# Performance work log

Measured on AMD Instinct MI355X. Metric: run time of the kernel, lower is better.

Reference implementation:

```python
import jax, jax.numpy as jnp
import numpy as np

LEAKY = 0.2  # tf.nn.leaky_relu default alpha
E_SZ = [64, 64, 16]
F_SZ = [128, 128, 8]
N_MAPS, C, H, W = 64, 1, 32, 32
B = 8192


def _leaky(x):
    return jnp.where(x >= 0, x, LEAKY * x)


def func_theta(x, theta, sz, in_sz):
    # x: [B, in_sz]; theta: [B, total]; per-sample MLP with weights sliced from theta
    y = x
    offset = 0
    n = len(sz)
    for i, out_sz in enumerate(sz):
        w_sz = in_sz * out_sz
        Wm = theta[:, offset:offset + w_sz].reshape(-1, in_sz, out_sz)
        offset += w_sz
        b = theta[:, offset:offset + out_sz]
        offset += out_sz
        y = jnp.einsum('bi,bio->bo', y, Wm) + b
        if i < n - 1:
            y = _leaky(y)
        in_sz = out_sz
    return y


def setup_inputs() -> dict:
    key = jax.random.key(0)
    ks = jax.random.split(key, 16)

    def g(k, shape, scale):
        return (jax.random.normal(k, shape, dtype=jnp.float32) * scale)

    inp = {
        'indices': jax.random.randint(ks[0], (B,), 0, N_MAPS, dtype=jnp.int32),
        'states': jax.random.normal(ks[1], (B, 4), dtype=jnp.float32),
        'maps': jax.random.normal(ks[2], (N_MAPS, C, H, W), dtype=jnp.float32),
        'fc1_w': g(ks[3], (C * H * W, 256), 1.0 / np.sqrt(C * H * W)),
        'fc1_b': jnp.zeros((256,), jnp.float32),
        'fc2_w': g(ks[4], (256, 128), 1.0 / np.sqrt(256)),
        'fc2_b': jnp.zeros((128,), jnp.float32),
        'fc3_w': g(ks[5], (128, 128), 1.0 / np.sqrt(128)),
        'fc3_b': jnp.zeros((128,), jnp.float32),
        'bn_w': g(ks[6], (128, 32), 1.0 / np.sqrt(128)),
        'bn_b': jnp.zeros((32,), jnp.float32),
        'e_w': g(ks[7], (32, 5456), 1e-5),
        'e_b': g(ks[8], (5456,), 1e-3),
        'f_w': g(ks[9], (32, 21768), 1e-5),
        'f_b': g(ks[10], (21768,), 1e-3),
    }
    return inp


def reference(indices, states, maps, fc1_w, fc1_b, fc2_w, fc2_b, fc3_w, fc3_b,
              bn_w, bn_b, e_w, e_b, f_w, f_b):
    # gather maps per sample and flatten (NCHW -> NHWC transpose is a no-op after flatten
    # mathematically, but keep the exact data layout of the original)
    m = jnp.transpose(maps[indices], (0, 2, 3, 1)).astype(jnp.float32)  # [B,H,W,C]
    z = m.reshape(m.shape[0], -1)

    # hypernet trunk
    z = _leaky(z @ fc1_w + fc1_b)
    z = _leaky(z @ fc2_w + fc2_b)
    z = _leaky(z @ fc3_w + fc3_b)
    z = z @ bn_w + bn_b  # bottleneck, no activation
    theta_e = z @ e_w + e_b  # [B, 5456]
    theta_f = z @ f_w + f_b  # [B, 21768]

    S = states[:, 0:2]
    G = states[:, 2:4]
    e_s = func_theta(S, theta_e, E_SZ, 2)
    e_g = func_theta(G, theta_e, E_SZ, 2)
    zf = jnp.concatenate([e_s, e_g], axis=-1)  # [B, 32]
    ang = func_theta(zf, theta_f, F_SZ, 2 * E_SZ[-1])  # [B, 8]
    pts = jnp.concatenate([jnp.sin(ang), jnp.cos(ang)], axis=-1)  # [B, 16]
    return pts
```

## Files before the change

### kernel.cpp

```cpp
#include <hip/hip_runtime.h>
#include <hip/hip_bf16.h>


#define LEAKY 0.2f
#define NCLS 64
#define B_TOT 8192
#define NSLICE 4


__device__ __forceinline__ float lrelu(float x) { return x >= 0.f ? x : LEAKY * x; }

__global__ __launch_bounds__(1024) void backbone_bucket_kernel(
    const float* __restrict__ maps,
    const float* __restrict__ fc1_w, const float* __restrict__ fc1_b,
    const float* __restrict__ fc2_w, const float* __restrict__ fc2_b,
    const float* __restrict__ fc3_w, const float* __restrict__ fc3_b,
    const float* __restrict__ bn_w,  const float* __restrict__ bn_b,
    float* __restrict__ z,
    const int* __restrict__ idx, int* __restrict__ counts,
    int* __restrict__ offsets, int* __restrict__ perm)
{
    __shared__ float m[1024];
    __shared__ float red[1024];
    __shared__ float h1[256];
    __shared__ float h2[128];
    __shared__ float h3[128];
    __shared__ int cnt[16][64];
    __shared__ int wcur[16][64];

    const int t = threadIdx.x;

    if (blockIdx.x == 64) {
        const int w = t >> 6;
        cnt[w][t & 63] = 0;
        __syncthreads();
        int my[8];
#pragma unroll
        for (int r = 0; r < 8; ++r) {
            my[r] = idx[r * 1024 + t];
            atomicAdd(&cnt[w][my[r]], 1);
        }
        __syncthreads();
        if (t < 64) {
            int run = 0;
#pragma unroll
            for (int w2 = 0; w2 < 16; ++w2) {
                const int v = cnt[w2][t];
                wcur[w2][t] = run;
                run += v;
            }
            counts[t] = run;
            int x = run;
            for (int d = 1; d < 64; d <<= 1) {
                const int y = __shfl_up(x, d, 64);
                if (t >= d) x += y;
            }
            const int basec = x - run;
            offsets[t] = basec;
#pragma unroll
            for (int w2 = 0; w2 < 16; ++w2) wcur[w2][t] += basec;
        }
        __syncthreads();
#pragma unroll
        for (int r = 0; r < 8; ++r) {
            const int p = atomicAdd(&wcur[w][my[r]], 1);
            perm[p] = r * 1024 + t;
        }
        return;
    }

    const int c = blockIdx.x;
    m[t] = maps[(size_t)c * 1024 + t];
    __syncthreads();

    {
        const int o = t & 255, ks = t >> 8;
        const float* wp = fc1_w + o;
        float acc = 0.f;
#pragma unroll 8
        for (int i = 0; i < 256; ++i) {
            const int k = ks * 256 + i;
            acc += m[k] * wp[(size_t)k * 256];
        }
        red[t] = acc;
    }
    __syncthreads();
    if (t < 256)
        h1[t] = lrelu(fc1_b[t] + red[t] + red[256 + t] + red[512 + t] + red[768 + t]);
    __syncthreads();
    {
        const int o = t & 127, ks = t >> 7;
        float acc = 0.f;
#pragma unroll
        for (int i = 0; i < 32; ++i) {
            const int k = ks * 32 + i;
            acc += h1[k] * fc2_w[k * 128 + o];
        }
        red[t] = acc;
    }
    __syncthreads();
    if (t < 128) {
        float a = fc2_b[t];
#pragma unroll
        for (int r = 0; r < 8; ++r) a += red[r * 128 + t];
        h2[t] = lrelu(a);
    }
    __syncthreads();
    {
        const int o = t & 127, ks = t >> 7;
        float acc = 0.f;
#pragma unroll
        for (int i = 0; i < 16; ++i) {
            const int k = ks * 16 + i;
            acc += h2[k] * fc3_w[k * 128 + o];
        }
        red[t] = acc;
    }
    __syncthreads();
    if (t < 128) {
        float a = fc3_b[t];
#pragma unroll
        for (int r = 0; r < 8; ++r) a += red[r * 128 + t];
        h3[t] = lrelu(a);
    }
    __syncthreads();
    {
        const int o = t & 31, ks = t >> 5;
        float acc = 0.f;
#pragma unroll
        for (int i = 0; i < 4; ++i) {
            const int k = ks * 4 + i;
            acc += h3[k] * bn_w[k * 32 + o];
        }
        red[t] = acc;
    }
    __syncthreads();
    if (t < 32) {
        float a = bn_b[t];
#pragma unroll
        for (int r = 0; r < 32; ++r) a += red[r * 32 + t];
        z[c * 32 + t] = a;
    }
}

__global__ __launch_bounds__(256) void theta_kernel(
    const float* __restrict__ z,
    const float* __restrict__ e_w, const float* __restrict__ e_b,
    const float* __restrict__ f_w, const float* __restrict__ f_b,
    float* __restrict__ th_e, float* __restrict__ th_f)
{
    __shared__ __align__(16) float zl[2048];
    const int t = threadIdx.x;
    ((float4*)zl)[t]       = ((const float4*)z)[t];
    ((float4*)zl)[t + 256] = ((const float4*)z)[t + 256];
    __syncthreads();

    int j = blockIdx.x * 256 + t;
    const int cbase = blockIdx.y * 8;
    const float* wbase;
    float* op;
    int stride;
    float bias;
    if (j < 5456) {
        wbase = e_w + j; bias = e_b[j]; op = th_e + j; stride = 5456;
    } else {
        const int jj = j - 5456;
        if (jj >= 21768) return;
        wbase = f_w + jj; bias = f_b[jj]; op = th_f + jj; stride = 21768;
    }
    float wk[32];
#pragma unroll
    for (int k = 0; k < 32; ++k) wk[k] = wbase[(size_t)k * stride];

#pragma unroll
    for (int cc = 0; cc < 8; cc += 4) {
        const int c0 = cbase + cc;
        float a0 = bias, a1 = bias, a2 = bias, a3 = bias;
#pragma unroll
        for (int k4 = 0; k4 < 8; ++k4) {
            const float4 z0 = *(const float4*)&zl[(c0 + 0) * 32 + k4 * 4];
            const float4 z1 = *(const float4*)&zl[(c0 + 1) * 32 + k4 * 4];
            const float4 z2 = *(const float4*)&zl[(c0 + 2) * 32 + k4 * 4];
            const float4 z3 = *(const float4*)&zl[(c0 + 3) * 32 + k4 * 4];
            const float w0 = wk[k4 * 4], w1 = wk[k4 * 4 + 1];
            const float w2 = wk[k4 * 4 + 2], w3 = wk[k4 * 4 + 3];
            a0 += z0.x * w0 + z0.y * w1 + z0.z * w2 + z0.w * w3;
            a1 += z1.x * w0 + z1.y * w1 + z1.z * w2 + z1.w * w3;
            a2 += z2.x * w0 + z2.y * w1 + z2.z * w2 + z2.w * w3;
            a3 += z3.x * w0 + z3.y * w1 + z3.z * w2 + z3.w * w3;
        }
        op[(size_t)(c0 + 0) * stride] = a0;
        op[(size_t)(c0 + 1) * stride] = a1;
        op[(size_t)(c0 + 2) * stride] = a2;
        op[(size_t)(c0 + 3) * stride] = a3;
    }
}

#define ESTRIDE 68
#define FSTRIDE 132

#define K3_LDS_FLOATS 35864
#define K3_LDS_BYTES  (K3_LDS_FLOATS * 4)

__global__ __launch_bounds__(512) void func_kernel(
    const float* __restrict__ states,
    const float* __restrict__ th_e_all, const float* __restrict__ th_f_all,
    const int* __restrict__ counts, const int* __restrict__ offsets,
    const int* __restrict__ perm, float* __restrict__ out)
{
    extern __shared__ float smem[];
    float* wE   = smem;
    float* wF   = smem + 5392;
    float* actA = smem + 27160;
    float* actB = smem + 31512;

    const int c = blockIdx.x;
    const int s = blockIdx.y;
    const int nb   = counts[c];
    const int base = offsets[c];
    const int nblk = (nb + 31) >> 5;
    const int npass = (nblk > s) ? ((nblk - 1 - s) / NSLICE + 1) : 0;
    if (npass == 0) return;

    const float* te = th_e_all + (size_t)c * 5456;
    const float* tf = th_f_all + (size_t)c * 21768;

    const int t  = threadIdx.x;
    const int b  = t & 31;
    const int ve = (t >> 5) & 1;
    const int vb = t & 63;
    const int ge = t >> 6;
    const int gf = t >> 5;
    const int cole = ge * 8;
    const int colf = gf * 8;
    const int eoff = vb * ESTRIDE;
    const int foff = b * FSTRIDE;

    for (int j = t * 4; j < 5392; j += 2048)
        *(float4*)&wE[j] = *(const float4*)&te[j];
    for (int j = t * 4; j < 21768; j += 2048)
        *(float4*)&wF[j] = *(const float4*)&tf[j];

    for (int p = 0; p < npass; ++p) {
        __syncthreads();

        const int kk = ((p * NSLICE + s) << 5) + b;
        const bool valid = kk < nb;
        const int bi = valid ? perm[base + kk] : 0;
        const float2 sv = *(const float2*)&states[(size_t)bi * 4 + 2 * ve];

        {
            const float4 wa0 = *(const float4*)&wE[cole];
            const float4 wa1 = *(const float4*)&wE[cole + 4];
            const float4 wb0 = *(const float4*)&wE[64 + cole];
            const float4 wb1 = *(const float4*)&wE[64 + cole + 4];
            const float4 bb0 = *(const float4*)&wE[128 + cole];
            const float4 bb1 = *(const float4*)&wE[128 + cole + 4];
            float4 o0, o1;
            o0.x = lrelu(sv.x * wa0.x + sv.y * wb0.x + bb0.x);
            o0.y = lrelu(sv.x * wa0.y + sv.y * wb0.y + bb0.y);
            o0.z = lrelu(sv.x * wa0.z + sv.y * wb0.z + bb0.z);
            o0.w = lrelu(sv.x * wa0.w + sv.y * wb0.w + bb0.w);
            o1.x = lrelu(sv.x * wa1.x + sv.y * wb1.x + bb1.x);
            o1.y = lrelu(sv.x * wa1.y + sv.y * wb1.y + bb1.y);
            o1.z = lrelu(sv.x * wa1.z + sv.y * wb1.z + bb1.z);
            o1.w = lrelu(sv.x * wa1.w + sv.y * wb1.w + bb1.w);
            *(float4*)&actA[eoff + cole]     = o0;
            *(float4*)&actA[eoff + cole + 4] = o1;
        }
        __syncthreads();

        {
            float acc[8] = {0, 0, 0, 0, 0, 0, 0, 0};
#pragma unroll 4
            for (int i4 = 0; i4 < 16; ++i4) {
                const float4 y4 = *(const float4*)&actA[eoff + i4 * 4];
#pragma unroll
                for (int u = 0; u < 4; ++u) {
                    const int row = 192 + (i4 * 4 + u) * 64 + cole;
                    const float4 wA = *(const float4*)&wE[row];
                    const float4 wB = *(const float4*)&wE[row + 4];
                    const float yv = (&y4.x)[u];
                    acc[0] += yv * wA.x; acc[1] += yv * wA.y;
                    acc[2] += yv * wA.z; acc[3] += yv * wA.w;
                    acc[4] += yv * wB.x; acc[5] += yv * wB.y;
                    acc[6] += yv * wB.z; acc[7] += yv * wB.w;
                }
            }
            const float4 bA = *(const float4*)&wE[4288 + cole];
            const float4 bB = *(const float4*)&wE[4288 + cole + 4];
            float4 o0, o1;
            o0.x = lrelu(acc[0] + bA.x); o0.y = lrelu(acc[1] + bA.y);
            o0.z = lrelu(acc[2] + bA.z); o0.w = lrelu(acc[3] + bA.w);
            o1.x = lrelu(acc[4] + bB.x); o1.y = lrelu(acc[5] + bB.y);
            o1.z = lrelu(acc[6] + bB.z); o1.w = lrelu(acc[7] + bB.w);
            *(float4*)&actB[eoff + cole]     = o0;
            *(float4*)&actB[eoff + cole + 4] = o1;
        }
        __syncthreads();

        {
            const int col3 = ge * 2;
            float a0 = 0.f, a1 = 0.f;
#pragma unroll 4
            for (int i4 = 0; i4 < 16; ++i4) {
                const float4 y4 = *(const float4*)&actB[eoff + i4 * 4];
#pragma unroll
                for (int u = 0; u < 4; ++u) {
                    const int i = i4 * 4 + u;
                    const float yv = (&y4.x)[u];
                    const float2 w2 = *(const float2*)&wE[4352 + i * 16 + col3];
                    a0 += yv * w2.x;
                    a1 += yv * w2.y;
                }
            }
            a0 += wE[5376 + col3];
            a1 += wE[5376 + col3 + 1];
            actA[foff + ve * 16 + col3]     = a0;
            actA[foff + ve * 16 + col3 + 1] = a1;
        }
        __syncthreads();

        {
            float acc[8] = {0, 0, 0, 0, 0, 0, 0, 0};
#pragma unroll
            for (int i4 = 0; i4 < 8; ++i4) {
                const float4 y4 = *(const float4*)&actA[foff + i4 * 4];
#pragma unroll
                for (int u = 0; u < 4; ++u) {
                    const int row = (i4 * 4 + u) * 128 + colf;
                    const float4 wA = *(const float4*)&wF[row];
                    const float4 wB = *(const float4*)&wF[row + 4];
                    const float yv = (&y4.x)[u];
                    acc[0] += yv * wA.x; acc[1] += yv * wA.y;
                    acc[2] += yv * wA.z; acc[3] += yv * wA.w;
                    acc[4] += yv * wB.x; acc[5] += yv * wB.y;
                    acc[6] += yv * wB.z; acc[7] += yv * wB.w;
                }
            }
            const float4 bA = *(const float4*)&wF[4096 + colf];
            const float4 bB = *(const float4*)&wF[4096 + colf + 4];
            float4 o0, o1;
            o0.x = lrelu(acc[0] + bA.x); o0.y = lrelu(acc[1] + bA.y);
            o0.z = lrelu(acc[2] + bA.z); o0.w = lrelu(acc[3] + bA.w);
            o1.x = lrelu(acc[4] + bB.x); o1.y = lrelu(acc[5] + bB.y);
            o1.z = lrelu(acc[6] + bB.z); o1.w = lrelu(acc[7] + bB.w);
            *(float4*)&actB[foff + colf]     = o0;
            *(float4*)&actB[foff + colf + 4] = o1;
        }
        __syncthreads();

        {
            float acc[8] = {0, 0, 0, 0, 0, 0, 0, 0};
#pragma unroll 4
            for (int i4 = 0; i4 < 32; ++i4) {
                const float4 y4 = *(const float4*)&actB[foff + i4 * 4];
#pragma unroll
                for (int u = 0; u < 4; ++u) {
                    const int row = 4224 + (i4 * 4 + u) * 128 + colf;
                    const float4 wA = *(const float4*)&wF[row];
                    const float4 wB = *(const float4*)&wF[row + 4];
                    const float yv = (&y4.x)[u];
                    acc[0] += yv * wA.x; acc[1] += yv * wA.y;
                    acc[2] += yv * wA.z; acc[3] += yv * wA.w;
                    acc[4] += yv * wB.x; acc[5] += yv * wB.y;
                    acc[6] += yv * wB.z; acc[7] += yv * wB.w;
                }
            }
            const float4 bA = *(const float4*)&wF[20608 + colf];
            const float4 bB = *(const float4*)&wF[20608 + colf + 4];
            float4 o0, o1;
            o0.x = lrelu(acc[0] + bA.x); o0.y = lrelu(acc[1] + bA.y);
            o0.z = lrelu(acc[2] + bA.z); o0.w = lrelu(acc[3] + bA.w);
            o1.x = lrelu(acc[4] + bB.x); o1.y = lrelu(acc[5] + bB.y);
            o1.z = lrelu(acc[6] + bB.z); o1.w = lrelu(acc[7] + bB.w);
            *(float4*)&actA[foff + colf]     = o0;
            *(float4*)&actA[foff + colf + 4] = o1;
        }
        __syncthreads();

        if (gf < 8) {
            float a = 0.f;
#pragma unroll 8
            for (int i4 = 0; i4 < 32; ++i4) {
                const float4 y4 = *(const float4*)&actA[foff + i4 * 4];
#pragma unroll
                for (int u = 0; u < 4; ++u)
                    a += (&y4.x)[u] * wF[20736 + (i4 * 4 + u) * 8 + gf];
            }
            a += wF[21760 + gf];
            if (valid) {
                out[(size_t)bi * 16 + gf]     = __sinf(a);
                out[(size_t)bi * 16 + 8 + gf] = __cosf(a);
            }
        }
    }
}

extern "C" void kernel_launch(void* const* d_in, const int* in_sizes, int n_in,
                              void* d_out, int out_size, void* d_ws, size_t ws_size,
                              hipStream_t stream)
{
    const int*   indices = (const int*)  d_in[0];
    const float* states  = (const float*)d_in[1];
    const float* maps    = (const float*)d_in[2];
    const float* fc1_w   = (const float*)d_in[3];
    const float* fc1_b   = (const float*)d_in[4];
    const float* fc2_w   = (const float*)d_in[5];
    const float* fc2_b   = (const float*)d_in[6];
    const float* fc3_w   = (const float*)d_in[7];
    const float* fc3_b   = (const float*)d_in[8];
    const float* bn_w    = (const float*)d_in[9];
    const float* bn_b    = (const float*)d_in[10];
    const float* e_w     = (const float*)d_in[11];
    const float* e_b     = (const float*)d_in[12];
    const float* f_w     = (const float*)d_in[13];
    const float* f_b     = (const float*)d_in[14];
    float* out = (float*)d_out;

    float* ws   = (float*)d_ws;
    float* z    = ws;
    float* th_e = ws + 2048;
    float* th_f = ws + 351232;
    int* counts  = (int*)(ws + 1744384);
    int* offsets = counts + 64;
    int* perm    = counts + 128;

    static int s_lds_optin = 0;
    if (!s_lds_optin) {
        hipFuncSetAttribute((const void*)func_kernel,
                            hipFuncAttributeMaxDynamicSharedMemorySize,
                            K3_LDS_BYTES);
        s_lds_optin = 1;
    }

    backbone_bucket_kernel<<<65, 1024, 0, stream>>>(
        maps, fc1_w, fc1_b, fc2_w, fc2_b, fc3_w, fc3_b, bn_w, bn_b, z,
        indices, counts, offsets, perm);
    theta_kernel<<<dim3(107, 8), 256, 0, stream>>>(
        z, e_w, e_b, f_w, f_b, th_e, th_f);
    func_kernel<<<dim3(NCLS, NSLICE), 512, K3_LDS_BYTES, stream>>>(
        states, th_e, th_f, counts, offsets, perm, out);
}
```

Before: 139.7 us.

## Split fc1 into wider-grid kernel and double samples per func_kernel pass

Moves the fc1 layer out of the backbone into its own kernel with 256 blocks (4 output quarters per map class), so the 4 MB weight read is spread over more CUs than the 64 backbone blocks could use. The per-sample func_kernel now processes 64 samples per pass, with two accumulator sets per thread, so each LDS weight load is reused twice. The large F hidden-layer weights are streamed through a smaller LDS buffer in two halves per pass instead of being held whole. NSLICE drops to 3. The cost is an extra kernel launch, higher register pressure, and repeated global reloads of the middle weight matrix on every pass.

```diff
diff --git a/kernel.cpp b/kernel.cpp
--- a/kernel.cpp
+++ b/kernel.cpp
@@ -5,14 +5,45 @@
 #define LEAKY 0.2f
 #define NCLS 64
 #define B_TOT 8192
-#define NSLICE 4
+#define NSLICE 3
 
 
 __device__ __forceinline__ float lrelu(float x) { return x >= 0.f ? x : LEAKY * x; }
 
+__global__ __launch_bounds__(1024) void fc1_kernel(
+    const float* __restrict__ maps, const float* __restrict__ fc1_w,
+    const float* __restrict__ fc1_b, float* __restrict__ h1g)
+{
+    __shared__ float m[1024];
+    __shared__ float red[1024];
+    const int t = threadIdx.x;
+    const int c = blockIdx.x >> 2;
+    const int q = blockIdx.x & 3;
+
+    m[t] = maps[(size_t)c * 1024 + t];
+    __syncthreads();
+
+    const int ol = t & 63, ks = t >> 6;
+    const int o = q * 64 + ol;
+    const float* wp = fc1_w + o;
+    float acc = 0.f;
+#pragma unroll 8
+    for (int i = 0; i < 64; ++i) {
+        const int k = ks * 64 + i;
+        acc += m[k] * wp[(size_t)k * 256];
+    }
+    red[t] = acc;
+    __syncthreads();
+    if (t < 64) {
+        float a = fc1_b[q * 64 + t];
+#pragma unroll
+        for (int r = 0; r < 16; ++r) a += red[r * 64 + t];
+        h1g[c * 256 + q * 64 + t] = lrelu(a);
+    }
+}
+
 __global__ __launch_bounds__(1024) void backbone_bucket_kernel(
-    const float* __restrict__ maps,
-    const float* __restrict__ fc1_w, const float* __restrict__ fc1_b,
+    const float* __restrict__ h1g,
     const float* __restrict__ fc2_w, const float* __restrict__ fc2_b,
     const float* __restrict__ fc3_w, const float* __restrict__ fc3_b,
     const float* __restrict__ bn_w,  const float* __restrict__ bn_b,
@@ -20,7 +51,6 @@
     const int* __restrict__ idx, int* __restrict__ counts,
     int* __restrict__ offsets, int* __restrict__ perm)
 {
-    __shared__ float m[1024];
     __shared__ float red[1024];
     __shared__ float h1[256];
     __shared__ float h2[128];
@@ -70,24 +100,9 @@
     }
 
     const int c = blockIdx.x;
-    m[t] = maps[(size_t)c * 1024 + t];
-    __syncthreads();
-
-    {
-        const int o = t & 255, ks = t >> 8;
-        const float* wp = fc1_w + o;
-        float acc = 0.f;
-#pragma unroll 8
-        for (int i = 0; i < 256; ++i) {
-            const int k = ks * 256 + i;
-            acc += m[k] * wp[(size_t)k * 256];
-        }
-        red[t] = acc;
-    }
-    __syncthreads();
-    if (t < 256)
-        h1[t] = lrelu(fc1_b[t] + red[t] + red[256 + t] + red[512 + t] + red[768 + t]);
-    __syncthreads();
+    if (t < 256) h1[t] = h1g[c * 256 + t];
+    __syncthreads();
+
     {
         const int o = t & 127, ks = t >> 7;
         float acc = 0.f;
@@ -199,7 +214,7 @@
 #define ESTRIDE 68
 #define FSTRIDE 132
 
-#define K3_LDS_FLOATS 35864
+#define K3_LDS_FLOATS 36376
 #define K3_LDS_BYTES  (K3_LDS_FLOATS * 4)
 
 __global__ __launch_bounds__(512) void func_kernel(
@@ -210,15 +225,16 @@
 {
     extern __shared__ float smem[];
     float* wE   = smem;
-    float* wF   = smem + 5392;
-    float* actA = smem + 27160;
-    float* actB = smem + 31512;
+    float* wFa  = smem + 5392;
+    float* wH   = smem + 10776;
+    float* actA = smem + 18968;
+    float* actB = smem + 27672;
 
     const int c = blockIdx.x;
     const int s = blockIdx.y;
     const int nb   = counts[c];
     const int base = offsets[c];
-    const int nblk = (nb + 31) >> 5;
+    const int nblk = (nb + 63) >> 6;
     const int npass = (nblk > s) ? ((nblk - 1 - s) / NSLICE + 1) : 0;
     if (npass == 0) return;
 
@@ -227,27 +243,33 @@
 
     const int t  = threadIdx.x;
     const int b  = t & 31;
-    const int ve = (t >> 5) & 1;
-    const int vb = t & 63;
+    const int v  = t & 63;
     const int ge = t >> 6;
     const int gf = t >> 5;
     const int cole = ge * 8;
     const int colf = gf * 8;
-    const int eoff = vb * ESTRIDE;
-    const int foff = b * FSTRIDE;
+    const int eoffL = v * ESTRIDE;
+    const int eoffH = (v + 64) * ESTRIDE;
+    const int foff0 = b * FSTRIDE;
+    const int foff1 = (b + 32) * FSTRIDE;
 
     for (int j = t * 4; j < 5392; j += 2048)
         *(float4*)&wE[j] = *(const float4*)&te[j];
-    for (int j = t * 4; j < 21768; j += 2048)
-        *(float4*)&wF[j] = *(const float4*)&tf[j];
+    for (int j = t * 4; j < 4224; j += 2048)
+        *(float4*)&wFa[j] = *(const float4*)&tf[j];
+    for (int j = t * 4; j < 1160; j += 2048)
+        *(float4*)&wFa[4224 + j] = *(const float4*)&tf[20608 + j];
 
     for (int p = 0; p < npass; ++p) {
         __syncthreads();
 
-        const int kk = ((p * NSLICE + s) << 5) + b;
-        const bool valid = kk < nb;
-        const int bi = valid ? perm[base + kk] : 0;
-        const float2 sv = *(const float2*)&states[(size_t)bi * 4 + 2 * ve];
+        for (int j = t * 4; j < 8192; j += 2048)
+            *(float4*)&wH[j] = *(const float4*)&tf[4224 + j];
+
+        const int kbase = (p * NSLICE + s) << 6;
+        const int ib_e  = kbase + v;
+        const int bi_e  = (ib_e < nb) ? perm[base + ib_e] : 0;
+        const float4 st = *(const float4*)&states[(size_t)bi_e * 4];
 
         {
             const float4 wa0 = *(const float4*)&wE[cole];
@@ -257,141 +279,224 @@
             const float4 bb0 = *(const float4*)&wE[128 + cole];
             const float4 bb1 = *(const float4*)&wE[128 + cole + 4];
             float4 o0, o1;
-            o0.x = lrelu(sv.x * wa0.x + sv.y * wb0.x + bb0.x);
-            o0.y = lrelu(sv.x * wa0.y + sv.y * wb0.y + bb0.y);
-            o0.z = lrelu(sv.x * wa0.z + sv.y * wb0.z + bb0.z);
-            o0.w = lrelu(sv.x * wa0.w + sv.y * wb0.w + bb0.w);
-            o1.x = lrelu(sv.x * wa1.x + sv.y * wb1.x + bb1.x);
-            o1.y = lrelu(sv.x * wa1.y + sv.y * wb1.y + bb1.y);
-            o1.z = lrelu(sv.x * wa1.z + sv.y * wb1.z + bb1.z);
-            o1.w = lrelu(sv.x * wa1.w + sv.y * wb1.w + bb1.w);
-            *(float4*)&actA[eoff + cole]     = o0;
-            *(float4*)&actA[eoff + cole + 4] = o1;
+            o0.x = lrelu(st.x * wa0.x + st.y * wb0.x + bb0.x);
+            o0.y = lrelu(st.x * wa0.y + st.y * wb0.y + bb0.y);
+            o0.z = lrelu(st.x * wa0.z + st.y * wb0.z + bb0.z);
+            o0.w = lrelu(st.x * wa0.w + st.y * wb0.w + bb0.w);
+            o1.x = lrelu(st.x * wa1.x + st.y * wb1.x + bb1.x);
+            o1.y = lrelu(st.x * wa1.y + st.y * wb1.y + bb1.y);
+            o1.z = lrelu(st.x * wa1.z + st.y * wb1.z + bb1.z);
+            o1.w = lrelu(st.x * wa1.w + st.y * wb1.w + bb1.w);
+            *(float4*)&actA[eoffL + cole]     = o0;
+            *(float4*)&actA[eoffL + cole + 4] = o1;
+            o0.x = lrelu(st.z * wa0.x + st.w * wb0.x + bb0.x);
+            o0.y = lrelu(st.z * wa0.y + st.w * wb0.y + bb0.y);
+            o0.z = lrelu(st.z * wa0.z + st.w * wb0.z + bb0.z);
+            o0.w = lrelu(st.z * wa0.w + st.w * wb0.w + bb0.w);
+            o1.x = lrelu(st.z * wa1.x + st.w * wb1.x + bb1.x);
+            o1.y = lrelu(st.z * wa1.y + st.w * wb1.y + bb1.y);
+            o1.z = lrelu(st.z * wa1.z + st.w * wb1.z + bb1.z);
+            o1.w = lrelu(st.z * wa1.w + st.w * wb1.w + bb1.w);
+            *(float4*)&actA[eoffH + cole]     = o0;
+            *(float4*)&actA[eoffH + cole + 4] = o1;
         }
         __syncthreads();
 
         {
-            float acc[8] = {0, 0, 0, 0, 0, 0, 0, 0};
+            float aL[8] = {0,0,0,0,0,0,0,0};
+            float aH[8] = {0,0,0,0,0,0,0,0};
 #pragma unroll 4
             for (int i4 = 0; i4 < 16; ++i4) {
-                const float4 y4 = *(const float4*)&actA[eoff + i4 * 4];
+                const float4 yL = *(const float4*)&actA[eoffL + i4 * 4];
+                const float4 yH = *(const float4*)&actA[eoffH + i4 * 4];
 #pragma unroll
                 for (int u = 0; u < 4; ++u) {
                     const int row = 192 + (i4 * 4 + u) * 64 + cole;
                     const float4 wA = *(const float4*)&wE[row];
                     const float4 wB = *(const float4*)&wE[row + 4];
-                    const float yv = (&y4.x)[u];
-                    acc[0] += yv * wA.x; acc[1] += yv * wA.y;
-                    acc[2] += yv * wA.z; acc[3] += yv * wA.w;
-                    acc[4] += yv * wB.x; acc[5] += yv * wB.y;
-                    acc[6] += yv * wB.z; acc[7] += yv * wB.w;
+                    const float yl = (&yL.x)[u], yh = (&yH.x)[u];
+                    aL[0] += yl * wA.x; aL[1] += yl * wA.y;
+                    aL[2] += yl * wA.z; aL[3] += yl * wA.w;
+                    aL[4] += yl * wB.x; aL[5] += yl * wB.y;
+                    aL[6] += yl * wB.z; aL[7] += yl * wB.w;
+                    aH[0] += yh * wA.x; aH[1] += yh * wA.y;
+                    aH[2] += yh * wA.z; aH[3] += yh * wA.w;
+                    aH[4] += yh * wB.x; aH[5] += yh * wB.y;
+                    aH[6] += yh * wB.z; aH[7] += yh * wB.w;
                 }
             }
             const float4 bA = *(const float4*)&wE[4288 + cole];
             const float4 bB = *(const float4*)&wE[4288 + cole + 4];
             float4 o0, o1;
-            o0.x = lrelu(acc[0] + bA.x); o0.y = lrelu(acc[1] + bA.y);
-            o0.z = lrelu(acc[2] + bA.z); o0.w = lrelu(acc[3] + bA.w);
-            o1.x = lrelu(acc[4] + bB.x); o1.y = lrelu(acc[5] + bB.y);
-            o1.z = lrelu(acc[6] + bB.z); o1.w = lrelu(acc[7] + bB.w);
-            *(float4*)&actB[eoff + cole]     = o0;
-            *(float4*)&actB[eoff + cole + 4] = o1;
+            o0.x = lrelu(aL[0] + bA.x); o0.y = lrelu(aL[1] + bA.y);
+            o0.z = lrelu(aL[2] + bA.z); o0.w = lrelu(aL[3] + bA.w);
+            o1.x = lrelu(aL[4] + bB.x); o1.y = lrelu(aL[5] + bB.y);
+            o1.z = lrelu(aL[6] + bB.z); o1.w = lrelu(aL[7] + bB.w);
+            *(float4*)&actB[eoffL + cole]     = o0;
+            *(float4*)&actB[eoffL + cole + 4] = o1;
+            o0.x = lrelu(aH[0] + bA.x); o0.y = lrelu(aH[1] + bA.y);
+            o0.z = lrelu(aH[2] + bA.z); o0.w = lrelu(aH[3] + bA.w);
+            o1.x = lrelu(aH[4] + bB.x); o1.y = lrelu(aH[5] + bB.y);
+            o1.z = lrelu(aH[6] + bB.z); o1.w = lrelu(aH[7] + bB.w);
+            *(float4*)&actB[eoffH + cole]     = o0;
+            *(float4*)&actB[eoffH + cole + 4] = o1;
         }
         __syncthreads();
 
         {
             const int col3 = ge * 2;
-            float a0 = 0.f, a1 = 0.f;
+            float a0 = 0.f, a1 = 0.f, a2 = 0.f, a3 = 0.f;
 #pragma unroll 4
             for (int i4 = 0; i4 < 16; ++i4) {
-                const float4 y4 = *(const float4*)&actB[eoff + i4 * 4];
+                const float4 yL = *(const float4*)&actB[eoffL + i4 * 4];
+                const float4 yH = *(const float4*)&actB[eoffH + i4 * 4];
 #pragma unroll
                 for (int u = 0; u < 4; ++u) {
-                    const int i = i4 * 4 + u;
-                    const float yv = (&y4.x)[u];
-                    const float2 w2 = *(const float2*)&wE[4352 + i * 16 + col3];
-                    a0 += yv * w2.x;
-                    a1 += yv * w2.y;
+                    const float2 w2 = *(const float2*)&wE[4352 + (i4 * 4 + u) * 16 + col3];
+                    const float yl = (&yL.x)[u], yh = (&yH.x)[u];
+                    a0 += yl * w2.x; a1 += yl * w2.y;
+                    a2 += yh * w2.x; a3 += yh * w2.y;
                 }
             }
-            a0 += wE[5376 + col3];
-            a1 += wE[5376 + col3 + 1];
-            actA[foff + ve * 16 + col3]     = a0;
-            actA[foff + ve * 16 + col3 + 1] = a1;
+            const float b0 = wE[5376 + col3], b1 = wE[5376 + col3 + 1];
+            actA[v * FSTRIDE + col3]          = a0 + b0;
+            actA[v * FSTRIDE + col3 + 1]      = a1 + b1;
+            actA[v * FSTRIDE + 16 + col3]     = a2 + b0;
+            actA[v * FSTRIDE + 16 + col3 + 1] = a3 + b1;
         }
         __syncthreads();
 
         {
-            float acc[8] = {0, 0, 0, 0, 0, 0, 0, 0};
+            float a0[8] = {0,0,0,0,0,0,0,0};
+            float a1[8] = {0,0,0,0,0,0,0,0};
 #pragma unroll
             for (int i4 = 0; i4 < 8; ++i4) {
-                const float4 y4 = *(const float4*)&actA[foff + i4 * 4];
+                const float4 y0 = *(const float4*)&actA[foff0 + i4 * 4];
+                const float4 y1 = *(const float4*)&actA[foff1 + i4 * 4];
 #pragma unroll
                 for (int u = 0; u < 4; ++u) {
                     const int row = (i4 * 4 + u) * 128 + colf;
-                    const float4 wA = *(const float4*)&wF[row];
-                    const float4 wB = *(const float4*)&wF[row + 4];
-                    const float yv = (&y4.x)[u];
-                    acc[0] += yv * wA.x; acc[1] += yv * wA.y;
-                    acc[2] += yv * wA.z; acc[3] += yv * wA.w;
-                    acc[4] += yv * wB.x; acc[5] += yv * wB.y;
-                    acc[6] += yv * wB.z; acc[7] += yv * wB.w;
+                    const float4 wA = *(const float4*)&wFa[row];
+                    const float4 wB = *(const float4*)&wFa[row + 4];
+                    const float ya = (&y0.x)[u], yb = (&y1.x)[u];
+                    a0[0] += ya * wA.x; a0[1] += ya * wA.y;
+                    a0[2] += ya * wA.z; a0[3] += ya * wA.w;
+                    a0[4] += ya * wB.x; a0[5] += ya * wB.y;
+                    a0[6] += ya * wB.z; a0[7] += ya * wB.w;
+                    a1[0] += yb * wA.x; a1[1] += yb * wA.y;
+                    a1[2] += yb * wA.z; a1[3] += yb * wA.w;
+                    a1[4] += yb * wB.x; a1[5] += yb * wB.y;
+                    a1[6] += yb * wB.z; a1[7] += yb * wB.w;
                 }
             }
-            const float4 bA = *(const float4*)&wF[4096 + colf];
-            const float4 bB = *(const float4*)&wF[4096 + colf + 4];
+            const float4 bA = *(const float4*)&wFa[4096 + colf];
+            const float4 bB = *(const float4*)&wFa[4096 + colf + 4];
             float4 o0, o1;
-            o0.x = lrelu(acc[0] + bA.x); o0.y = lrelu(acc[1] + bA.y);
-            o0.z = lrelu(acc[2] + bA.z); o0.w = lrelu(acc[3] + bA.w);
-            o1.x = lrelu(acc[4] + bB.x); o1.y = lrelu(acc[5] + bB.y);
-            o1.z = lrelu(acc[6] + bB.z); o1.w = lrelu(acc[7] + bB.w);
-            *(float4*)&actB[foff + colf]     = o0;
-            *(float4*)&actB[foff + colf + 4] = o1;
+            o0.x = lrelu(a0[0] + bA.x); o0.y = lrelu(a0[1] + bA.y);
+            o0.z = lrelu(a0[2] + bA.z); o0.w = lrelu(a0[3] + bA.w);
+            o1.x = lrelu(a0[4] + bB.x); o1.y = lrelu(a0[5] + bB.y);
+            o1.z = lrelu(a0[6] + bB.z); o1.w = lrelu(a0[7] + bB.w);
+            *(float4*)&actB[foff0 + colf]     = o0;
+            *(float4*)&actB[foff0 + colf + 4] = o1;
+            o0.x = lrelu(a1[0] + bA.x); o0.y = lrelu(a1[1] + bA.y);
+            o0.z = lrelu(a1[2] + bA.z); o0.w = lrelu(a1[3] + bA.w);
+            o1.x = lrelu(a1[4] + bB.x); o1.y = lrelu(a1[5] + bB.y);
+            o1.z = lrelu(a1[6] + bB.z); o1.w = lrelu(a1[7] + bB.w);
+            *(float4*)&actB[foff1 + colf]     = o0;
+            *(float4*)&actB[foff1 + colf + 4] = o1;
         }
         __syncthreads();
 
         {
-            float acc[8] = {0, 0, 0, 0, 0, 0, 0, 0};
+            float a0[8] = {0,0,0,0,0,0,0,0};
+            float a1[8] = {0,0,0,0,0,0,0,0};
 #pragma unroll 4
-            for (int i4 = 0; i4 < 32; ++i4) {
-                const float4 y4 = *(const float4*)&actB[foff + i4 * 4];
+            for (int i4 = 0; i4 < 16; ++i4) {
+                const float4 y0 = *(const float4*)&actB[foff0 + i4 * 4];
+                const float4 y1 = *(const float4*)&actB[foff1 + i4 * 4];
 #pragma unroll
                 for (int u = 0; u < 4; ++u) {
-                    const int row = 4224 + (i4 * 4 + u) * 128 + colf;
-                    const float4 wA = *(const float4*)&wF[row];
-                    const float4 wB = *(const float4*)&wF[row + 4];
-                    const float yv = (&y4.x)[u];
-                    acc[0] += yv * wA.x; acc[1] += yv * wA.y;
-                    acc[2] += yv * wA.z; acc[3] += yv * wA.w;
-                    acc[4] += yv * wB.x; acc[5] += yv * wB.y;
-                    acc[6] += yv * wB.z; acc[7] += yv * wB.w;
+                    const int row = (i4 * 4 + u) * 128 + colf;
+                    const float4 wA = *(const float4*)&wH[row];
+                    const float4 wB = *(const float4*)&wH[row + 4];
+                    const float ya = (&y0.x)[u], yb = (&y1.x)[u];
+                    a0[0] += ya * wA.x; a0[1] += ya * wA.y;
+                    a0[2] += ya * wA.z; a0[3] += ya * wA.w;
+                    a0[4] += ya * wB.x; a0[5] += ya * wB.y;
+                    a0[6] += ya * wB.z; a0[7] += ya * wB.w;
+                    a1[0] += yb * wA.x; a1[1] += yb * wA.y;
+                    a1[2] += yb * wA.z; a1[3] += yb * wA.w;
+                    a1[4] += yb * wB.x; a1[5] += yb * wB.y;
+                    a1[6] += yb * wB.z; a1[7] += yb * wB.w;
                 }
             }
-            const float4 bA = *(const float4*)&wF[20608 + colf];
-            const float4 bB = *(const float4*)&wF[20608 + colf + 4];
+            __syncthreads();
+            for (int j = t * 4; j < 8192; j += 2048)
+                *(float4*)&wH[j] = *(const float4*)&tf[4224 + 8192 + j];
+            __syncthreads();
+#pragma unroll 4
+            for (int i4 = 0; i4 < 16; ++i4) {
+                const float4 y0 = *(const float4*)&actB[foff0 + 64 + i4 * 4];
+                const float4 y1 = *(const float4*)&actB[foff1 + 64 + i4 * 4];
+#pragma unroll
+                for (int u = 0; u < 4; ++u) {
+                    const int row = (i4 * 4 + u) * 128 + colf;
+                    const float4 wA = *(const float4*)&wH[row];
+                    const float4 wB = *(const float4*)&wH[row + 4];
+                    const float ya = (&y0.x)[u], yb = (&y1.x)[u];
+                    a0[0] += ya * wA.x; a0[1] += ya * wA.y;
+                    a0[2] += ya * wA.z; a0[3] += ya * wA.w;
+                    a0[4] += ya * wB.x; a0[5] += ya * wB.y;
+                    a0[6] += ya * wB.z; a0[7] += ya * wB.w;
+                    a1[0] += yb * wA.x; a1[1] += yb * wA.y;
+                    a1[2] += yb * wA.z; a1[3] += yb * wA.w;
+                    a1[4] += yb * wB.x; a1[5] += yb * wB.y;
+                    a1[6] += yb * wB.z; a1[7] += yb * wB.w;
+                }
+            }
+            const float4 bA = *(const float4*)&wFa[4224 + colf];
+            const float4 bB = *(const float4*)&wFa[4224 + colf + 4];
             float4 o0, o1;
-            o0.x = lrelu(acc[0] + bA.x); o0.y = lrelu(acc[1] + bA.y);
-            o0.z = lrelu(acc[2] + bA.z); o0.w = lrelu(acc[3] + bA.w);
-            o1.x = lrelu(acc[4] + bB.x); o1.y = lrelu(acc[5] + bB.y);
-            o1.z = lrelu(acc[6] + bB.z); o1.w = lrelu(acc[7] + bB.w);
-            *(float4*)&actA[foff + colf]     = o0;
-            *(float4*)&actA[foff + colf + 4] = o1;
+            o0.x = lrelu(a0[0] + bA.x); o0.y = lrelu(a0[1] + bA.y);
+            o0.z = lrelu(a0[2] + bA.z); o0.w = lrelu(a0[3] + bA.w);
+            o1.x = lrelu(a0[4] + bB.x); o1.y = lrelu(a0[5] + bB.y);
+            o1.z = lrelu(a0[6] + bB.z); o1.w = lrelu(a0[7] + bB.w);
+            *(float4*)&actA[foff0 + colf]     = o0;
+            *(float4*)&actA[foff0 + colf + 4] = o1;
+            o0.x = lrelu(a1[0] + bA.x); o0.y = lrelu(a1[1] + bA.y);
+            o0.z = lrelu(a1[2] + bA.z); o0.w = lrelu(a1[3] + bA.w);
+            o1.x = lrelu(a1[4] + bB.x); o1.y = lrelu(a1[5] + bB.y);
+            o1.z = lrelu(a1[6] + bB.z); o1.w = lrelu(a1[7] + bB.w);
+            *(float4*)&actA[foff1 + colf]     = o0;
+            *(float4*)&actA[foff1 + colf + 4] = o1;
         }
         __syncthreads();
 
         if (gf < 8) {
-            float a = 0.f;
+            float a0 = 0.f, a1 = 0.f;
 #pragma unroll 8
             for (int i4 = 0; i4 < 32; ++i4) {
-                const float4 y4 = *(const float4*)&actA[foff + i4 * 4];
-#pragma unroll
-                for (int u = 0; u < 4; ++u)
-                    a += (&y4.x)[u] * wF[20736 + (i4 * 4 + u) * 8 + gf];
-            }
-            a += wF[21760 + gf];
-            if (valid) {
-                out[(size_t)bi * 16 + gf]     = __sinf(a);
-                out[(size_t)bi * 16 + 8 + gf] = __cosf(a);
+                const float4 y0 = *(const float4*)&actA[foff0 + i4 * 4];
+                const float4 y1 = *(const float4*)&actA[foff1 + i4 * 4];
+#pragma unroll
+                for (int u = 0; u < 4; ++u) {
+                    const float w = wFa[4352 + (i4 * 4 + u) * 8 + gf];
+                    a0 += (&y0.x)[u] * w;
+                    a1 += (&y1.x)[u] * w;
+                }
+            }
+            const float bb = wFa[5376 + gf];
+            a0 += bb; a1 += bb;
+            const int ib0 = kbase + b, ib1 = kbase + b + 32;
+            if (ib0 < nb) {
+                const int bi = perm[base + ib0];
+                out[(size_t)bi * 16 + gf]     = __sinf(a0);
+                out[(size_t)bi * 16 + 8 + gf] = __cosf(a0);
+            }
+            if (ib1 < nb) {
+                const int bi = perm[base + ib1];
+                out[(size_t)bi * 16 + gf]     = __sinf(a1);
+                out[(size_t)bi * 16 + 8 + gf] = __cosf(a1);
             }
         }
     }
@@ -425,6 +530,7 @@
     int* counts  = (int*)(ws + 1744384);
     int* offsets = counts + 64;
     int* perm    = counts + 128;
+    float* h1g   = ws + 1752704;
 
     static int s_lds_optin = 0;
     if (!s_lds_optin) {
@@ -434,8 +540,9 @@
         s_lds_optin = 1;
     }
 
+    fc1_kernel<<<256, 1024, 0, stream>>>(maps, fc1_w, fc1_b, h1g);
     backbone_bucket_kernel<<<65, 1024, 0, stream>>>(
-        maps, fc1_w, fc1_b, fc2_w, fc2_b, fc3_w, fc3_b, bn_w, bn_b, z,
+        h1g, fc2_w, fc2_b, fc3_w, fc3_b, bn_w, bn_b, z,
         indices, counts, offsets, perm);
     theta_kernel<<<dim3(107, 8), 256, 0, stream>>>(
         z, e_w, e_b, f_w, f_b, th_e, th_f);
```

Result: faster. 130.7 us (-6.4%).
